# Performance work log

Measured on AMD Instinct MI355X. Metric: run time of the kernel, lower is better.

## Reference

```python
import jax, jax.numpy as jnp
import numpy as np

V, C, L, NH, NKV, HID, E, K, T, B = 32000, 1536, 2, 12, 4, 2048, 8, 2, 2048, 1
D = C // NH  # 128
NREP = NH // NKV
EPS = 1e-6

def _rms(x, w):
    return x * jax.lax.rsqrt(jnp.mean(x * x, axis=-1, keepdims=True) + EPS) * w


def setup_inputs() -> dict:
    key = jax.random.key(0)
    ks = jax.random.split(key, 14)
    s = 0.02
    inp = {
        "tokens": jax.random.randint(ks[0], (B, T), 0, V, dtype=jnp.int64),
        "emb": jax.random.normal(ks[1], (V, C), jnp.float32) * s,      # tied with output proj
        "pos": jax.random.normal(ks[2], (T, C), jnp.float32) * s,
        "wq": jax.random.normal(ks[3], (L, C, NH * D), jnp.float32) * s,
        "wk": jax.random.normal(ks[4], (L, C, NKV * D), jnp.float32) * s,
        "wv": jax.random.normal(ks[5], (L, C, NKV * D), jnp.float32) * s,
        "wo": jax.random.normal(ks[6], (L, C, C), jnp.float32) * s,
        "attn_norm_w": jnp.ones((L, C), jnp.float32),
        "ffn_norm_w": jnp.ones((L, C), jnp.float32),
        "gate": jax.random.normal(ks[7], (L, C, E), jnp.float32) * s,
        "ew1": jax.random.normal(ks[8], (L, E, C, HID), jnp.float32) * s,
        "ew2": jax.random.normal(ks[9], (L, E, HID, C), jnp.float32) * s,
        "ew3": jax.random.normal(ks[10], (L, E, C, HID), jnp.float32) * s,
        "final_norm_w": jnp.ones((C,), jnp.float32),
    }
    return inp


def _forward(tokens, emb, pos, wq, wk, wv, wo, attn_norm_w, ffn_norm_w, gate,
             ew1, ew2, ew3, final_norm_w):
    x = emb[tokens] + pos[None, :T]            # [B,T,C]; dropout=0 (eval)
    causal = jnp.tril(jnp.ones((T, T), bool))
    for l in range(L):
        # --- GQA attention ---
        h = _rms(x, attn_norm_w[l])
        q = (h @ wq[l]).reshape(B, T, NH, D).transpose(0, 2, 1, 3)     # [B,NH,T,D]
        k = (h @ wk[l]).reshape(B, T, NKV, D).transpose(0, 2, 1, 3)
        v = (h @ wv[l]).reshape(B, T, NKV, D).transpose(0, 2, 1, 3)
        k = jnp.repeat(k, NREP, axis=1)
        v = jnp.repeat(v, NREP, axis=1)
        scores = jnp.einsum("bhqd,bhkd->bhqk", q, k) / jnp.sqrt(jnp.float32(D))
        scores = jnp.where(causal, scores, jnp.finfo(scores.dtype).min)
        attn = jax.nn.softmax(scores, axis=-1)
        y = jnp.einsum("bhqk,bhkd->bhqd", attn, v)
        y = y.transpose(0, 2, 1, 3).reshape(B, T, C)
        x = x + y @ wo[l]
        # --- MoE FFN (top-k routed SwiGLU experts) ---
        xf = _rms(x, ffn_norm_w[l]).reshape(-1, C)                      # [N,C]
        probs = jax.nn.softmax(xf @ gate[l], axis=-1)                   # [N,E]
        topw, topi = jax.lax.top_k(probs, K)
        topw = topw / jnp.sum(topw, axis=-1, keepdims=True)
        dense_w = jnp.sum(jax.nn.one_hot(topi, E, dtype=xf.dtype) * topw[..., None], axis=1)  # [N,E]
        h1 = jnp.einsum("nc,ech->enh", xf, ew1[l])
        h3 = jnp.einsum("nc,ech->enh", xf, ew3[l])
        hh = jax.nn.silu(h1) * h3                                       # [E,N,HID]
        moe = jnp.einsum("ne,enh,ehc->nc", dense_w, hh, ew2[l])
        x = x + moe.reshape(B, T, C)
    x = _rms(x, final_norm_w)
    logits = x @ emb.T                                                   # tied output proj
    return logits


def reference(tokens, emb, pos, wq, wk, wv, wo, attn_norm_w, ffn_norm_w, gate,
              ew1, ew2, ew3, final_norm_w):
    return _forward(tokens, emb, pos, wq, wk, wv, wo, attn_norm_w, ffn_norm_w,
                    gate, ew1, ew2, ew3, final_norm_w)
```

## Files before the change

### kernel.cpp

```cpp
#include <hip/hip_runtime.h>
#include <hip/hip_bf16.h>
#include <math.h>

#define Tn   2048
#define Cn   1536
#define Vn   32000
#define NHn  12
#define NKVn 4
#define Dn   128
#define HIDn 2048
#define En   8
#define Kn   2
#define Ln   2
#define NREPn 3
#define EPSn 1e-6f
#define CHT  16
#define NCHn 4
#define QKVW 2560

using bf16 = __hip_bfloat16;
using bf16x8 = __attribute__((ext_vector_type(8))) short;
using f32x4v = __attribute__((ext_vector_type(4))) float;

__device__ __forceinline__ void split3(float v, short& h, short& m, short& lo) {
  bf16 b0 = __float2bfloat16(v);
  float r1 = v - __bfloat162float(b0);
  bf16 b1 = __float2bfloat16(r1);
  float r2 = r1 - __bfloat162float(b1);
  bf16 b2 = __float2bfloat16(r2);
  h = *reinterpret_cast<short*>(&b0);
  m = *reinterpret_cast<short*>(&b1);
  lo = *reinterpret_cast<short*>(&b2);
}
__device__ __forceinline__ float b2f(short s) {
  bf16 b = *reinterpret_cast<bf16*>(&s);
  return __bfloat162float(b);
}
__device__ __forceinline__ void gl_lds16(const void* g, void* l) {
  __builtin_amdgcn_global_load_lds((const __attribute__((address_space(1))) void*)g,
                                   (__attribute__((address_space(3))) void*)l, 16, 0, 0);
}

__global__ void embed_k(const int* __restrict__ tok, const float* __restrict__ emb,
                        const float* __restrict__ pos, float* __restrict__ x) {
  int n = blockIdx.x;
  int t = threadIdx.x;
  int id = tok[n];
  const float* er = emb + (size_t)id * Cn;
  const float* pr = pos + (size_t)n * Cn;
// ... 37 lines not shown
  const float* xr = x + (size_t)n * Cn;
  float v[6];
  float ss = 0.f;
#pragma unroll
  for (int i = 0; i < 6; i++) { v[i] = xr[t + i * 256]; ss += v[i] * v[i]; }
  for (int off = 32; off > 0; off >>= 1) ss += __shfl_down(ss, off, 64);
  __shared__ float red[4];
  __shared__ float rtot;
  int wave = t >> 6, lane = t & 63;
  if (lane == 0) red[wave] = ss;
  __syncthreads();
  if (t == 0) rtot = rsqrtf((red[0] + red[1] + red[2] + red[3]) / (float)Cn + EPSn);
  __syncthreads();
  float r = rtot;
#pragma unroll
  for (int i = 0; i < 6; i++) {
    int c = t + i * 256;
    float val = v[i] * r * w[c];
    size_t idx = (size_t)n * Cn + c;
    if (outf) outf[idx] = val;
    outb[idx] = __float2bfloat16(val);
  }
}

__global__ void f2b_k(const float* __restrict__ s, bf16* __restrict__ d, size_t n4) {
  size_t i = (size_t)blockIdx.x * 256 + threadIdx.x;
  size_t stride = (size_t)gridDim.x * 256;
  for (; i < n4; i += stride) {
    float4 v = ((const float4*)s)[i];
    d[i * 4 + 0] = __float2bfloat16(v.x);
    d[i * 4 + 1] = __float2bfloat16(v.y);
    d[i * 4 + 2] = __float2bfloat16(v.z);
    d[i * 4 + 3] = __float2bfloat16(v.w);
  }
}

__global__ void splita_k(const float* __restrict__ s, short* __restrict__ dh,
                         short* __restrict__ dm, short* __restrict__ dl, size_t n4) {
  size_t i = (size_t)blockIdx.x * 256 + threadIdx.x;
  size_t stride = (size_t)gridDim.x * 256;
  for (; i < n4; i += stride) {
    float4 v = ((const float4*)s)[i];
    float a[4] = {v.x, v.y, v.z, v.w};
#pragma unroll
    for (int u = 0; u < 4; u++) {
      short h, m, lo;
      split3(a[u], h, m, lo);
      dh[i * 4 + u] = h; dm[i * 4 + u] = m; dl[i * 4 + u] = lo;
    }
  }
}

__global__ void transp3_k(const float* __restrict__ src, short* __restrict__ dh,
                          short* __restrict__ dm, short* __restrict__ dl, int K, int N) {
  __shared__ __align__(16) float ls[32][33];
  size_t boff = (size_t)blockIdx.z * K * N;
  int k0 = blockIdx.x * 32, n0 = blockIdx.y * 32;
  int t = threadIdx.x;
  int kr = t >> 3, n4 = (t & 7) * 4;
  float4 vv = *(const float4*)&src[boff + (size_t)(k0 + kr) * N + n0 + n4];
  ls[kr][n4 + 0] = vv.x; ls[kr][n4 + 1] = vv.y; ls[kr][n4 + 2] = vv.z; ls[kr][n4 + 3] = vv.w;
  __syncthreads();
  int nr = t >> 3, k4 = (t & 7) * 4;
  size_t dbase = boff + (size_t)(n0 + nr) * K + k0 + k4;
#pragma unroll
  for (int u = 0; u < 4; u++) {
    short h, m, lo;
    split3(ls[k4 + u][nr], h, m, lo);
    dh[dbase + u] = h; dm[dbase + u] = m; dl[dbase + u] = lo;
  }
}

__global__ void transp_k(const float* __restrict__ src, bf16* __restrict__ dst, int K, int N) {
  __shared__ __align__(16) float ls[32][33];
  size_t boff = (size_t)blockIdx.z * K * N;
  int k0 = blockIdx.x * 32, n0 = blockIdx.y * 32;
  int t = threadIdx.x;
  int kr = t >> 3, n4 = (t & 7) * 4;
  float4 vv = *(const float4*)&src[boff + (size_t)(k0 + kr) * N + n0 + n4];
  ls[kr][n4 + 0] = vv.x; ls[kr][n4 + 1] = vv.y; ls[kr][n4 + 2] = vv.z; ls[kr][n4 + 3] = vv.w;
  __syncthreads();
  int nr = t >> 3, k4 = (t & 7) * 4;
// ... 106 lines not shown
      int ro = (wc + j * 16 + rl) * 32 + ko;
      bf16x8 bh = *(const bf16x8*)(sBH + ro);
      bf16x8 bm_ = *(const bf16x8*)(sBM + ro);
      bf16x8 bl = *(const bf16x8*)(sBL + ro);
#pragma unroll
      for (int i = 0; i < 4; i++) {
        acc[i][j] = __builtin_amdgcn_mfma_f32_16x16x32_bf16(aL[i], bh, acc[i][j], 0, 0, 0);
        acc[i][j] = __builtin_amdgcn_mfma_f32_16x16x32_bf16(aH[i], bl, acc[i][j], 0, 0, 0);
        acc[i][j] = __builtin_amdgcn_mfma_f32_16x16x32_bf16(aM[i], bm_, acc[i][j], 0, 0, 0);
        acc[i][j] = __builtin_amdgcn_mfma_f32_16x16x32_bf16(aM[i], bh, acc[i][j], 0, 0, 0);
        acc[i][j] = __builtin_amdgcn_mfma_f32_16x16x32_bf16(aH[i], bm_, acc[i][j], 0, 0, 0);
        acc[i][j] = __builtin_amdgcn_mfma_f32_16x16x32_bf16(aH[i], bh, acc[i][j], 0, 0, 0);
      }
    }
    __syncthreads();
  }
#pragma unroll
  for (int i = 0; i < 4; i++) {
    int rbase = bm + wr + i * 16 + (l >> 4) * 4;
#pragma unroll
    for (int j = 0; j < 4; j++) {
      int col = bn + wc + j * 16 + (l & 15);
#pragma unroll
      for (int r = 0; r < 4; r++) {
        size_t idx = (size_t)(rbase + r) * N + col;
        float v = acc[i][j][r];
        if (res) v += res[idx];
        Co[idx] = v;
      }
    }
  }
}

__global__ void __launch_bounds__(256) mexp6d(const bf16* __restrict__ AH, const bf16* __restrict__ AM,
                                              const bf16* __restrict__ AL,
                                              const bf16* __restrict__ B1H, const bf16* __restrict__ B1M,
                                              const bf16* __restrict__ B1L,
                                              const bf16* __restrict__ B3H, const bf16* __restrict__ B3M,
                                              const bf16* __restrict__ B3L,
                                              const int* __restrict__ perm, const int* __restrict__ cnt,
                                              int ebase,
                                              short* __restrict__ HH, short* __restrict__ HM,
                                              short* __restrict__ HL, int K, int N) {
  int e = ebase + blockIdx.z;
  int nrows = cnt[e];
  int bm = blockIdx.x * 128;
  if (bm >= nrows) return;
  int bn = blockIdx.y * 128;
  size_t eoff = (size_t)blockIdx.z * K * N;
  __shared__ __align__(16) bf16 sAH[128 * 32], sAM[128 * 32], sAL[128 * 32];
  __shared__ __align__(16) bf16 s1H[128 * 32], s1M[128 * 32], s1L[128 * 32];
  __shared__ __align__(16) bf16 s3H[128 * 32], s3M[128 * 32], s3L[128 * 32];
  __shared__ int prow[128];
  int t = threadIdx.x, l = t & 63, w = t >> 6;
  if (t < 128) {
    int i = bm + t;
    prow[t] = (i < nrows) ? perm[e * Tn + i] : -1;
  }
  __syncthreads();
  int wr = (w >> 1) * 64, wc = (w & 1) * 64;
  const f32x4v zero = {0.f, 0.f, 0.f, 0.f};
  f32x4v acc1[4][4], acc3[4][4];
#pragma unroll
  for (int i = 0; i < 4; i++)
#pragma unroll
    for (int j = 0; j < 4; j++) { acc1[i][j] = zero; acc3[i][j] = zero; }
  int p0 = prow[t >> 2], p1 = prow[64 + (t >> 2)];
  int g0r = (p0 >= 0) ? (p0 >> 1) : 0;
  int g1r = (p1 >= 0) ? (p1 >> 1) : 0;
  size_t a0 = (size_t)g0r * K + (t & 3) * 8;
  size_t a1 = (size_t)g1r * K + (t & 3) * 8;
  size_t b0 = eoff + (size_t)(bn + (t >> 2)) * K + (t & 3) * 8;
  size_t b1 = eoff + (size_t)(bn + 64 + (t >> 2)) * K + (t & 3) * 8;
  int rl = l & 15, ko = (l >> 4) * 8;
  for (int k0 = 0; k0 < K; k0 += 32) {
    gl_lds16(AH + a0 + k0, (char*)sAH + t * 16);
    gl_lds16(AH + a1 + k0, (char*)sAH + (256 + t) * 16);
    gl_lds16(AM + a0 + k0, (char*)sAM + t * 16);
    gl_lds16(AM + a1 + k0, (char*)sAM + (256 + t) * 16);
    gl_lds16(AL + a0 + k0, (char*)sAL + t * 16);
    gl_lds16(AL + a1 + k0, (char*)sAL + (256 + t) * 16);
    gl_lds16(B1H + b0 + k0, (char*)s1H + t * 16);
    gl_lds16(B1H + b1 + k0, (char*)s1H + (256 + t) * 16);
    gl_lds16(B1M + b0 + k0, (char*)s1M + t * 16);
    gl_lds16(B1M + b1 + k0, (char*)s1M + (256 + t) * 16);
    gl_lds16(B1L + b0 + k0, (char*)s1L + t * 16);
    gl_lds16(B1L + b1 + k0, (char*)s1L + (256 + t) * 16);
    gl_lds16(B3H + b0 + k0, (char*)s3H + t * 16);
    gl_lds16(B3H + b1 + k0, (char*)s3H + (256 + t) * 16);
    gl_lds16(B3M + b0 + k0, (char*)s3M + t * 16);
    gl_lds16(B3M + b1 + k0, (char*)s3M + (256 + t) * 16);
    gl_lds16(B3L + b0 + k0, (char*)s3L + t * 16);
    gl_lds16(B3L + b1 + k0, (char*)s3L + (256 + t) * 16);
    __syncthreads();
    bf16x8 aH[4], aM[4], aL[4];
#pragma unroll
    for (int i = 0; i < 4; i++) {
      int ro = (wr + i * 16 + rl) * 32 + ko;
      aH[i] = *(const bf16x8*)(sAH + ro);
      aM[i] = *(const bf16x8*)(sAM + ro);
      aL[i] = *(const bf16x8*)(sAL + ro);
    }
#pragma unroll
    for (int j = 0; j < 4; j++) {
      int ro = (wc + j * 16 + rl) * 32 + ko;
      bf16x8 bh = *(const bf16x8*)(s1H + ro);
      bf16x8 bm_ = *(const bf16x8*)(s1M + ro);
      bf16x8 bl = *(const bf16x8*)(s1L + ro);
#pragma unroll
      for (int i = 0; i < 4; i++) {
        acc1[i][j] = __builtin_amdgcn_mfma_f32_16x16x32_bf16(aL[i], bh, acc1[i][j], 0, 0, 0);
        acc1[i][j] = __builtin_amdgcn_mfma_f32_16x16x32_bf16(aH[i], bl, acc1[i][j], 0, 0, 0);
        acc1[i][j] = __builtin_amdgcn_mfma_f32_16x16x32_bf16(aM[i], bm_, acc1[i][j], 0, 0, 0);
        acc1[i][j] = __builtin_amdgcn_mfma_f32_16x16x32_bf16(aM[i], bh, acc1[i][j], 0, 0, 0);
        acc1[i][j] = __builtin_amdgcn_mfma_f32_16x16x32_bf16(aH[i], bm_, acc1[i][j], 0, 0, 0);
        acc1[i][j] = __builtin_amdgcn_mfma_f32_16x16x32_bf16(aH[i], bh, acc1[i][j], 0, 0, 0);
      }
      bh = *(const bf16x8*)(s3H + ro);
      bm_ = *(const bf16x8*)(s3M + ro);
      bl = *(const bf16x8*)(s3L + ro);
#pragma unroll
      for (int i = 0; i < 4; i++) {
        acc3[i][j] = __builtin_amdgcn_mfma_f32_16x16x32_bf16(aL[i], bh, acc3[i][j], 0, 0, 0);
        acc3[i][j] = __builtin_amdgcn_mfma_f32_16x16x32_bf16(aH[i], bl, acc3[i][j], 0, 0, 0);
        acc3[i][j] = __builtin_amdgcn_mfma_f32_16x16x32_bf16(aM[i], bm_, acc3[i][j], 0, 0, 0);
        acc3[i][j] = __builtin_amdgcn_mfma_f32_16x16x32_bf16(aM[i], bh, acc3[i][j], 0, 0, 0);
        acc3[i][j] = __builtin_amdgcn_mfma_f32_16x16x32_bf16(aH[i], bm_, acc3[i][j], 0, 0, 0);
        acc3[i][j] = __builtin_amdgcn_mfma_f32_16x16x32_bf16(aH[i], bh, acc3[i][j], 0, 0, 0);
      }
    }
    __syncthreads();
  }
#pragma unroll
  for (int i = 0; i < 4; i++) {
#pragma unroll
    for (int r = 0; r < 4; r++) {
      int lrow = wr + i * 16 + (l >> 4) * 4 + r;
      int p = prow[lrow];
      if (p < 0) continue;
#pragma unroll
      for (int j = 0; j < 4; j++) {
        int col = bn + wc + j * 16 + (l & 15);
        size_t idx = (size_t)p * N + col;
        float h1 = acc1[i][j][r], h3 = acc3[i][j][r];
        float hh = (h1 / (1.f + expf(-h1))) * h3;
        short h, m, lo;
        split3(hh, h, m, lo);
        HH[idx] = h; HM[idx] = m; HL[idx] = lo;
      }
    }
  }
}

__global__ void __launch_bounds__(256) mexp6(const bf16* __restrict__ AH, const bf16* __restrict__ AM,
                                             const bf16* __restrict__ AL,
                                             const bf16* __restrict__ BH, const bf16* __restrict__ BM,
                                             const bf16* __restrict__ BL,
                                             const int* __restrict__ perm, const int* __restrict__ cnt,
                                             int ebase, float* __restrict__ Co, int K, int N) {
  int e = ebase + blockIdx.z;
  int nrows = cnt[e];
  int bm = blockIdx.x * 128;
  if (bm >= nrows) return;
  int bn = blockIdx.y * 128;
  size_t eoff = (size_t)blockIdx.z * K * N;
  __shared__ __align__(16) bf16 sAH[128 * 32], sAM[128 * 32], sAL[128 * 32];
  __shared__ __align__(16) bf16 sBH[128 * 32], sBM[128 * 32], sBL[128 * 32];
  __shared__ int prow[128];
  int t = threadIdx.x, l = t & 63, w = t >> 6;
  if (t < 128) {
    int i = bm + t;
    prow[t] = (i < nrows) ? perm[e * Tn + i] : -1;
  }
  __syncthreads();
  int wr = (w >> 1) * 64, wc = (w & 1) * 64;
  const f32x4v zero = {0.f, 0.f, 0.f, 0.f};
  f32x4v acc[4][4];
#pragma unroll
  for (int i = 0; i < 4; i++)
#pragma unroll
    for (int j = 0; j < 4; j++) acc[i][j] = zero;
  int p0 = prow[t >> 2], p1 = prow[64 + (t >> 2)];
  int g0r = (p0 >= 0) ? p0 : 0;
  int g1r = (p1 >= 0) ? p1 : 0;
  size_t a0 = (size_t)g0r * K + (t & 3) * 8;
  size_t a1 = (size_t)g1r * K + (t & 3) * 8;
  size_t b0 = eoff + (size_t)(bn + (t >> 2)) * K + (t & 3) * 8;
  size_t b1 = eoff + (size_t)(bn + 64 + (t >> 2)) * K + (t & 3) * 8;
  int rl = l & 15, ko = (l >> 4) * 8;
  for (int k0 = 0; k0 < K; k0 += 32) {
    gl_lds16(AH + a0 + k0, (char*)sAH + t * 16);
    gl_lds16(AH + a1 + k0, (char*)sAH + (256 + t) * 16);
    gl_lds16(AM + a0 + k0, (char*)sAM + t * 16);
    gl_lds16(AM + a1 + k0, (char*)sAM + (256 + t) * 16);
    gl_lds16(AL + a0 + k0, (char*)sAL + t * 16);
    gl_lds16(AL + a1 + k0, (char*)sAL + (256 + t) * 16);
    gl_lds16(BH + b0 + k0, (char*)sBH + t * 16);
    gl_lds16(BH + b1 + k0, (char*)sBH + (256 + t) * 16);
    gl_lds16(BM + b0 + k0, (char*)sBM + t * 16);
    gl_lds16(BM + b1 + k0, (char*)sBM + (256 + t) * 16);
    gl_lds16(BL + b0 + k0, (char*)sBL + t * 16);
    gl_lds16(BL + b1 + k0, (char*)sBL + (256 + t) * 16);
    __syncthreads();
    bf16x8 aH[4], aM[4], aL[4];
#pragma unroll
    for (int i = 0; i < 4; i++) {
      int ro = (wr + i * 16 + rl) * 32 + ko;
      aH[i] = *(const bf16x8*)(sAH + ro);
      aM[i] = *(const bf16x8*)(sAM + ro);
      aL[i] = *(const bf16x8*)(sAL + ro);
    }
#pragma unroll
    for (int j = 0; j < 4; j++) {
      int ro = (wc + j * 16 + rl) * 32 + ko;
      bf16x8 bh = *(const bf16x8*)(sBH + ro);
      bf16x8 bm_ = *(const bf16x8*)(sBM + ro);
      bf16x8 bl = *(const bf16x8*)(sBL + ro);
#pragma unroll
      for (int i = 0; i < 4; i++) {
        acc[i][j] = __builtin_amdgcn_mfma_f32_16x16x32_bf16(aL[i], bh, acc[i][j], 0, 0, 0);
        acc[i][j] = __builtin_amdgcn_mfma_f32_16x16x32_bf16(aH[i], bl, acc[i][j], 0, 0, 0);
        acc[i][j] = __builtin_amdgcn_mfma_f32_16x16x32_bf16(aM[i], bm_, acc[i][j], 0, 0, 0);
        acc[i][j] = __builtin_amdgcn_mfma_f32_16x16x32_bf16(aM[i], bh, acc[i][j], 0, 0, 0);
        acc[i][j] = __builtin_amdgcn_mfma_f32_16x16x32_bf16(aH[i], bm_, acc[i][j], 0, 0, 0);
        acc[i][j] = __builtin_amdgcn_mfma_f32_16x16x32_bf16(aH[i], bh, acc[i][j], 0, 0, 0);
      }
    }
    __syncthreads();
  }
#pragma unroll
  for (int i = 0; i < 4; i++) {
#pragma unroll
    for (int r = 0; r < 4; r++) {
      int lrow = wr + i * 16 + (l >> 4) * 4 + r;
      int p = prow[lrow];
      if (p < 0) continue;
#pragma unroll
      for (int j = 0; j < 4; j++) {
        int col = bn + wc + j * 16 + (l & 15);
        Co[(size_t)p * N + col] = acc[i][j][r];
      }
    }
  }
}

__global__ void __launch_bounds__(256) mexpBd(const bf16* __restrict__ A, const bf16* __restrict__ B1,
                                              const bf16* __restrict__ B3,
                                              const int* __restrict__ perm, const int* __restrict__ cnt,
                                              int ebase, bf16* __restrict__ HB, int K, int N) {
  int e = ebase + blockIdx.z;
  int nrows = cnt[e];
  int bm = blockIdx.x * 128;
  if (bm >= nrows) return;
  int bn = blockIdx.y * 128;
  size_t eoff = (size_t)blockIdx.z * K * N;
  __shared__ __align__(16) bf16 sA[128 * 32];
  __shared__ __align__(16) bf16 s1[128 * 32];
  __shared__ __align__(16) bf16 s3[128 * 32];
  __shared__ int prow[128];
  int t = threadIdx.x, l = t & 63, w = t >> 6;
  if (t < 128) {
    int i = bm + t;
    prow[t] = (i < nrows) ? perm[e * Tn + i] : -1;
  }
  __syncthreads();
  int wr = (w >> 1) * 64, wc = (w & 1) * 64;
  const f32x4v zero = {0.f, 0.f, 0.f, 0.f};
  f32x4v acc1[4][4], acc3[4][4];
#pragma unroll
  for (int i = 0; i < 4; i++)
#pragma unroll
    for (int j = 0; j < 4; j++) { acc1[i][j] = zero; acc3[i][j] = zero; }
  int p0 = prow[t >> 2], p1 = prow[64 + (t >> 2)];
// ... 90 lines not shown
#pragma unroll
    for (int j = 0; j < 4; j++) b[j] = *(const bf16x8*)(sB + (wc + j * 16 + rl) * 32 + ko);
#pragma unroll
    for (int i = 0; i < 4; i++)
#pragma unroll
      for (int j = 0; j < 4; j++)
        acc[i][j] = __builtin_amdgcn_mfma_f32_16x16x32_bf16(a[i], b[j], acc[i][j], 0, 0, 0);
    __syncthreads();
  }
#pragma unroll
  for (int i = 0; i < 4; i++) {
#pragma unroll
    for (int r = 0; r < 4; r++) {
      int lrow = wr + i * 16 + (l >> 4) * 4 + r;
      int p = prow[lrow];
      if (p < 0) continue;
#pragma unroll
      for (int j = 0; j < 4; j++) {
        int col = bn + wc + j * 16 + (l & 15);
        Co[(size_t)p * N + col] = acc[i][j][r];
      }
    }
  }
}

__global__ void __launch_bounds__(256) attn_part_k(const float* __restrict__ qkv,
                                                   float* __restrict__ po,
                                                   float* __restrict__ pm,
                                                   float* __restrict__ pl) {
  int qt = blockIdx.x;
  int head = blockIdx.y;
  int ch = blockIdx.z;
  int ntiles = qt + 1;
  int tA = ch * CHT;
  if (tA >= ntiles) return;
  int tB = tA + CHT < ntiles ? tA + CHT : ntiles;
  int kvh = head / NREPn;
  int q0 = qt * 32;
  int t = threadIdx.x;
  int r = t >> 3, g = t & 7, d0 = g * 16;
  int row = q0 + r;
  __shared__ __align__(16) float ks[32][Dn + 4];
  __shared__ __align__(16) float vs[32][Dn + 4];
  const float scale = 0.08838834764831845f;
  float qr[16];
  {
    const float* qrow = qkv + (size_t)row * QKVW + head * Dn + d0;
#pragma unroll
    for (int j = 0; j < 16; j += 4) {
      float4 u = *(const float4*)(qrow + j);
      qr[j] = u.x * scale; qr[j + 1] = u.y * scale;
      qr[j + 2] = u.z * scale; qr[j + 3] = u.w * scale;
    }
  }
  float o[16];
#pragma unroll
  for (int j = 0; j < 16; j++) o[j] = 0.f;
  float rowm = -1e30f, rowl = 0.f;

  for (int kt = tA; kt < tB; kt++) {
    int kv0 = kt * 32;
    for (int e = t; e < 32 * 32; e += 256) {
      int rr = e >> 5, c4 = (e & 31) * 4;
      size_t base = (size_t)(kv0 + rr) * QKVW + kvh * Dn + c4;
      *(float4*)&ks[rr][c4] = *(const float4*)(qkv + base + 1536);
      *(float4*)&vs[rr][c4] = *(const float4*)(qkv + base + 2048);
    }
    __syncthreads();
    float s[32];
#pragma unroll
    for (int kk = 0; kk < 32; kk++) {
      const float* krow = &ks[kk][d0];
      float p = 0.f;
#pragma unroll
// ... 5 lines not shown
      p += __shfl_xor(p, 2);
      p += __shfl_xor(p, 4);
      s[kk] = p;
    }
    if (kt == qt) {
#pragma unroll
      for (int kk = 0; kk < 32; kk++)
        if (kk > r) s[kk] = -1e30f;
    }
    float mx = s[0];
#pragma unroll
    for (int kk = 1; kk < 32; kk++) mx = fmaxf(mx, s[kk]);
    float m_new = fmaxf(rowm, mx);
    float corr = expf(rowm - m_new);
    float sum = 0.f;
#pragma unroll
    for (int kk = 0; kk < 32; kk++) { s[kk] = expf(s[kk] - m_new); sum += s[kk]; }
    rowl = rowl * corr + sum;
    rowm = m_new;
#pragma unroll
    for (int j = 0; j < 16; j++) o[j] *= corr;
#pragma unroll
    for (int kk = 0; kk < 32; kk++) {
      float p = s[kk];
      const float* vrow = &vs[kk][d0];
#pragma unroll
      for (int j = 0; j < 16; j += 4) {
        float4 u = *(const float4*)(vrow + j);
        o[j] += p * u.x; o[j + 1] += p * u.y; o[j + 2] += p * u.z; o[j + 3] += p * u.w;
      }
    }
    __syncthreads();
  }
  size_t pidx = ((size_t)head * Tn + row) * NCHn + ch;
  if (g == 0) { pm[pidx] = rowm; pl[pidx] = rowl; }
  float* porow = po + pidx * Dn + d0;
#pragma unroll
  for (int j = 0; j < 16; j += 4) {
    float4 u;
    u.x = o[j]; u.y = o[j + 1]; u.z = o[j + 2]; u.w = o[j + 3];
    *(float4*)(porow + j) = u;
  }
}

__global__ void __launch_bounds__(256) attn_merge_k(const float* __restrict__ po,
                                                    const float* __restrict__ pm,
                                                    const float* __restrict__ pl,
                                                    float* __restrict__ y) {
  int qt = blockIdx.x;
  int head = blockIdx.y;
  int q0 = qt * 32;
  int t = threadIdx.x;
  int r = t >> 3, g = t & 7, d0 = g * 16;
  int row = q0 + r;
  int nach = (qt + CHT) / CHT;
  size_t base = ((size_t)head * Tn + row) * NCHn;
  float M = -1e30f;
  for (int c = 0; c < nach; c++) M = fmaxf(M, pm[base + c]);
  float L = 0.f;
  float acc[16];
#pragma unroll
  for (int j = 0; j < 16; j++) acc[j] = 0.f;
  for (int c = 0; c < nach; c++) {
    float wgt = expf(pm[base + c] - M);
    L += pl[base + c] * wgt;
    const float* p = po + (base + c) * Dn + d0;
#pragma unroll
    for (int j = 0; j < 16; j += 4) {
      float4 u = *(const float4*)(p + j);
      acc[j] += wgt * u.x; acc[j + 1] += wgt * u.y;
      acc[j + 2] += wgt * u.z; acc[j + 3] += wgt * u.w;
    }
  }
  float inv = 1.f / L;
  float* yrow = y + (size_t)row * (NHn * Dn) + head * Dn + d0;
#pragma unroll
  for (int j = 0; j < 16; j += 4) {
    float4 u;
    u.x = acc[j] * inv; u.y = acc[j + 1] * inv;
    u.z = acc[j + 2] * inv; u.w = acc[j + 3] * inv;
    *(float4*)(yrow + j) = u;
  }
}

__global__ void gate_k(const float* __restrict__ xf, const float* __restrict__ g,
                       float* __restrict__ gl) {
  int n = blockIdx.x, t = threadIdx.x;
  int e = t & 7, cs = t >> 3;
  const float* xr = xf + (size_t)n * Cn;
  float s = 0.f;
  for (int j = 0; j < Cn / 32; j++) {
    int c = cs + 32 * j;
    s += xr[c] * g[c * En + e];
  }
  __shared__ float red[256];
  red[t] = s;
  __syncthreads();
  if (t < 8) {
    float tot = 0.f;
    for (int j = 0; j < 32; j++) tot += red[t + 8 * j];
    gl[n * En + t] = tot;
  }
}

__global__ void route_k(const float* __restrict__ gl, float* __restrict__ topw,
                        int* __restrict__ cnt, int* __restrict__ perm) {
  int n = blockIdx.x * blockDim.x + threadIdx.x;
  if (n >= Tn) return;
  float p[En];
  float mx = -1e30f;
#pragma unroll
  for (int e = 0; e < En; e++) { p[e] = gl[n * En + e]; mx = fmaxf(mx, p[e]); }
  float s = 0.f;
#pragma unroll
// ... 52 lines not shown
    off = (off + 255) & ~(size_t)255;
    size_t p = off;
    off += bytes;
    return p;
  };
  size_t o_x    = alloc(NC * 4);
  size_t o_h    = alloc(NC * 4);
  size_t o_gl   = alloc((size_t)Tn * En * 4);
  size_t o_topw = alloc((size_t)Tn * Kn * 4);
  size_t o_cnt  = alloc(64);
  size_t o_perm = alloc((size_t)En * Tn * 4);
  size_t wlvl   = (size_t)4 * Cn * HIDn * 2;
  size_t o_w    = alloc(3 * wlvl);
  size_t hs_lvl = NC * 2;
  size_t o_hs   = alloc(3 * hs_lvl);
  size_t o_qkv  = alloc((size_t)Tn * QKVW * 4);
  size_t o_yb   = alloc(NC * 4);
  size_t hb_lvl = (size_t)Tn * Kn * HIDn * 2;
  size_t o_hbs  = o_qkv;
  size_t end_hbs = o_hbs + 3 * hb_lvl;
  if (off < end_hbs) off = end_hbs;
  size_t o_pair = alloc(NC * 4);
  size_t o_po   = alloc((size_t)NHn * Tn * NCHn * Dn * 4);
  size_t o_pm   = alloc((size_t)NHn * Tn * NCHn * 4);
  size_t o_pl   = alloc((size_t)NHn * Tn * NCHn * 4);

  float* x       = (float*)(wsb + o_x);
  float* h       = (float*)(wsb + o_h);
  float* gl      = (float*)(wsb + o_gl);
  float* topw    = (float*)(wsb + o_topw);
  int*   cnt     = (int*)(wsb + o_cnt);
  int*   perm    = (int*)(wsb + o_perm);
  float* qkvb    = (float*)(wsb + o_qkv);
  float* yb      = (float*)(wsb + o_yb);
  float* pairout = (float*)(wsb + o_pair);
  bf16*  hb      = (bf16*)(wsb + o_pair);
  bf16*  embB    = (bf16*)(wsb + o_w);
  float* po      = (float*)(wsb + o_po);
  float* pm      = (float*)(wsb + o_pm);
  float* pl      = (float*)(wsb + o_pl);

  short* hs[3]; short* hbs[3];
  for (int s = 0; s < 3; s++) {
    hs[s]  = (short*)(wsb + o_hs + (size_t)s * hs_lvl);
    hbs[s] = (short*)(wsb + o_hbs + (size_t)s * hb_lvl);
  }
  size_t qkvw_lvl = (size_t)QKVW * Cn * 2;
  size_t wo_lvl   = (size_t)Cn * Cn * 2;
  short* qkvT[3]; short* woT[3];
  for (int s = 0; s < 3; s++) {
    qkvT[s] = (short*)(wsb + o_w + (size_t)s * qkvw_lvl);
    woT[s]  = (short*)(wsb + o_w + 3 * qkvw_lvl + (size_t)s * wo_lvl);
  }
  size_t q2lvl = (size_t)2 * Cn * HIDn * 2;
  short* e1T[3]; short* e3T[3]; short* e2T[3];
  for (int s = 0; s < 3; s++) {
    e1T[s] = (short*)(wsb + o_w + (size_t)s * q2lvl);
    e3T[s] = (short*)(wsb + o_w + 3 * q2lvl + (size_t)s * q2lvl);
    e2T[s] = (short*)(wsb + o_w + (size_t)s * wlvl);
  }
  bf16* ew1B = (bf16*)(wsb + o_w);
  bf16* ew3B = (bf16*)(wsb + o_w + wlvl);
  bf16* ew2B = (bf16*)(wsb + o_w);

  embed_k<<<Tn, 256, 0, stream>>>(tokens, emb, pos, x);
  for (int l = 0; l < Ln; l++) {
    const float* wq_l = wq + (size_t)l * Cn * (NHn * Dn);
    const float* wk_l = wk + (size_t)l * Cn * (NKVn * Dn);
    const float* wv_l = wv + (size_t)l * Cn * (NKVn * Dn);
    const float* wo_l = wo + (size_t)l * Cn * Cn;
    const float* g_l  = gate + (size_t)l * Cn * En;
    const float* e1_l = ew1 + (size_t)l * En * Cn * HIDn;
    const float* e2_l = ew2 + (size_t)l * En * HIDn * Cn;
    const float* e3_l = ew3 + (size_t)l * En * Cn * HIDn;

    transp3_k<<<dim3(Cn / 32, (NHn * Dn) / 32, 1), 256, 0, stream>>>(wq_l, qkvT[0], qkvT[1], qkvT[2], Cn, NHn * Dn);
    transp3_k<<<dim3(Cn / 32, (NKVn * Dn) / 32, 1), 256, 0, stream>>>(
        wk_l, qkvT[0] + (size_t)1536 * Cn, qkvT[1] + (size_t)1536 * Cn, qkvT[2] + (size_t)1536 * Cn, Cn, NKVn * Dn);
    transp3_k<<<dim3(Cn / 32, (NKVn * Dn) / 32, 1), 256, 0, stream>>>(
        wv_l, qkvT[0] + (size_t)2048 * Cn, qkvT[1] + (size_t)2048 * Cn, qkvT[2] + (size_t)2048 * Cn, Cn, NKVn * Dn);
    transp3_k<<<dim3(Cn / 32, Cn / 32, 1), 256, 0, stream>>>(wo_l, woT[0], woT[1], woT[2], Cn, Cn);
    rms3_k<<<Tn, 256, 0, stream>>>(x, attn_nw + (size_t)l * Cn, nullptr, hs[0], hs[1], hs[2]);
    gemm6<<<dim3(Tn / 128, QKVW / 128), 256, 0, stream>>>(
        (bf16*)hs[0], (bf16*)hs[1], (bf16*)hs[2], (bf16*)qkvT[0], (bf16*)qkvT[1], (bf16*)qkvT[2],
        nullptr, qkvb, Tn, QKVW, Cn);
    attn_part_k<<<dim3(Tn / 32, NHn, NCHn), 256, 0, stream>>>(qkvb, po, pm, pl);
    attn_merge_k<<<dim3(Tn / 32, NHn), 256, 0, stream>>>(po, pm, pl, yb);
    splita_k<<<2048, 256, 0, stream>>>(yb, hs[0], hs[1], hs[2], NC / 4);
    gemm6<<<dim3(Tn / 128, Cn / 128), 256, 0, stream>>>(
        (bf16*)hs[0], (bf16*)hs[1], (bf16*)hs[2], (bf16*)woT[0], (bf16*)woT[1], (bf16*)woT[2],
        x, x, Tn, Cn, Cn);

    if (l < Ln - 1) {
      rms3_k<<<Tn, 256, 0, stream>>>(x, ffn_nw + (size_t)l * Cn, h, hs[0], hs[1], hs[2]);
      gate_k<<<Tn, 256, 0, stream>>>(h, g_l, gl);
      hipMemsetAsync(cnt, 0, 64, stream);
      route_k<<<Tn / 256, 256, 0, stream>>>(gl, topw, cnt, perm);
      for (int q = 0; q < 4; q++) {
        size_t qoff = (size_t)q * 2 * Cn * HIDn;
        transp3_k<<<dim3(Cn / 32, HIDn / 32, 2), 256, 0, stream>>>(e1_l + qoff, e1T[0], e1T[1], e1T[2], Cn, HIDn);
        transp3_k<<<dim3(Cn / 32, HIDn / 32, 2), 256, 0, stream>>>(e3_l + qoff, e3T[0], e3T[1], e3T[2], Cn, HIDn);
        mexp6d<<<dim3(Tn / 128, HIDn / 128, 2), 256, 0, stream>>>(
            (bf16*)hs[0], (bf16*)hs[1], (bf16*)hs[2],
            (bf16*)e1T[0], (bf16*)e1T[1], (bf16*)e1T[2],
            (bf16*)e3T[0], (bf16*)e3T[1], (bf16*)e3T[2],
            perm, cnt, q * 2, hbs[0], hbs[1], hbs[2], Cn, HIDn);
      }
      for (int half = 0; half < 2; half++) {
        size_t hoff = (size_t)half * 4 * HIDn * Cn;
        transp3_k<<<dim3(HIDn / 32, Cn / 32, 4), 256, 0, stream>>>(e2_l + hoff, e2T[0], e2T[1], e2T[2], HIDn, Cn);
        mexp6<<<dim3(Tn / 128, Cn / 128, 4), 256, 0, stream>>>(
            (bf16*)hbs[0], (bf16*)hbs[1], (bf16*)hbs[2], (bf16*)e2T[0], (bf16*)e2T[1], (bf16*)e2T[2],
            perm, cnt, half * 4, pairout, HIDn, Cn);
      }
    } else {
      bf16* hbf = (bf16*)hs[0];
      bf16* hbB = (bf16*)hbs[0];
      rmsb_k<<<Tn, 256, 0, stream>>>(x, ffn_nw + (size_t)l * Cn, h, hbf);
      gate_k<<<Tn, 256, 0, stream>>>(h, g_l, gl);
      hipMemsetAsync(cnt, 0, 64, stream);
      route_k<<<Tn / 256, 256, 0, stream>>>(gl, topw, cnt, perm);
      for (int half = 0; half < 2; half++) {
        size_t hoff = (size_t)half * 4 * Cn * HIDn;
        int eb = half * 4;
        transp_k<<<dim3(Cn / 32, HIDn / 32, 4), 256, 0, stream>>>(e1_l + hoff, ew1B, Cn, HIDn);
        transp_k<<<dim3(Cn / 32, HIDn / 32, 4), 256, 0, stream>>>(e3_l + hoff, ew3B, Cn, HIDn);
        mexpBd<<<dim3(Tn / 128, HIDn / 128, 4), 256, 0, stream>>>(
            hbf, ew1B, ew3B, perm, cnt, eb, hbB, Cn, HIDn);
        transp_k<<<dim3(HIDn / 32, Cn / 32, 4), 256, 0, stream>>>(e2_l + (size_t)half * 4 * HIDn * Cn, ew2B, HIDn, Cn);
        mexpB<<<dim3(Tn / 128, Cn / 128, 4), 256, 0, stream>>>(
            hbB, ew2B, perm, cnt, eb, pairout, HIDn, Cn);
      }
    }
    combine_k<<<Tn, 256, 0, stream>>>(pairout, topw, x);
  }
  rmsb_k<<<Tn, 256, 0, stream>>>(x, final_nw, nullptr, hb);
  f2b_k<<<2048, 256, 0, stream>>>(emb, embB, (size_t)Vn * Cn / 4);
  gemm_btl<<<dim3(Tn / 128, Vn / 128), 256, 0, stream>>>(hb, embB, nullptr, out, Tn, Vn, Cn);
}
```

Baseline: 5.360 ms.

## Split fused dual-GEMM expert kernel, rebalance attention chunks, fuse merge with split

Removes the fused W1/W3 expert kernel (mexp6d) and replaces it with two passes of a generalized mexp6 kernel. The first pass stores the split h1, and the second reads it back and applies SiLU gating in the epilogue. Expert processing moves from quarter groups of two experts to halves of four, so there are fewer transposes and larger launches, at the cost of an extra round trip of h1 through memory. Attention partial chunks are now balanced evenly across NCH splits instead of fixed 16-tile chunks. The attention merge writes the three-way bf16 split directly, removing the separate fp32 output buffer and the splita pass.

```diff
diff --git a/kernel.cpp b/kernel.cpp
--- a/kernel.cpp
+++ b/kernel.cpp
@@ -14,7 +14,6 @@
 #define Ln   2
 #define NREPn 3
 #define EPSn 1e-6f
-#define CHT  16
 #define NCHn 4
 #define QKVW 2560
 
@@ -118,22 +117,6 @@
     d[i * 4 + 1] = __float2bfloat16(v.y);
     d[i * 4 + 2] = __float2bfloat16(v.z);
     d[i * 4 + 3] = __float2bfloat16(v.w);
-  }
-}
-
-__global__ void splita_k(const float* __restrict__ s, short* __restrict__ dh,
-                         short* __restrict__ dm, short* __restrict__ dl, size_t n4) {
-  size_t i = (size_t)blockIdx.x * 256 + threadIdx.x;
-  size_t stride = (size_t)gridDim.x * 256;
-  for (; i < n4; i += stride) {
-    float4 v = ((const float4*)s)[i];
-    float a[4] = {v.x, v.y, v.z, v.w};
-#pragma unroll
-    for (int u = 0; u < 4; u++) {
-      short h, m, lo;
-      split3(a[u], h, m, lo);
-      dh[i * 4 + u] = h; dm[i * 4 + u] = m; dl[i * 4 + u] = lo;
-    }
   }
 }
 
@@ -306,132 +289,15 @@
   }
 }
 
-__global__ void __launch_bounds__(256) mexp6d(const bf16* __restrict__ AH, const bf16* __restrict__ AM,
-                                              const bf16* __restrict__ AL,
-                                              const bf16* __restrict__ B1H, const bf16* __restrict__ B1M,
-                                              const bf16* __restrict__ B1L,
-                                              const bf16* __restrict__ B3H, const bf16* __restrict__ B3M,
-                                              const bf16* __restrict__ B3L,
-                                              const int* __restrict__ perm, const int* __restrict__ cnt,
-                                              int ebase,
-                                              short* __restrict__ HH, short* __restrict__ HM,
-                                              short* __restrict__ HL, int K, int N) {
-  int e = ebase + blockIdx.z;
-  int nrows = cnt[e];
-  int bm = blockIdx.x * 128;
-  if (bm >= nrows) return;
-  int bn = blockIdx.y * 128;
-  size_t eoff = (size_t)blockIdx.z * K * N;
-  __shared__ __align__(16) bf16 sAH[128 * 32], sAM[128 * 32], sAL[128 * 32];
-  __shared__ __align__(16) bf16 s1H[128 * 32], s1M[128 * 32], s1L[128 * 32];
-  __shared__ __align__(16) bf16 s3H[128 * 32], s3M[128 * 32], s3L[128 * 32];
-  __shared__ int prow[128];
-  int t = threadIdx.x, l = t & 63, w = t >> 6;
-  if (t < 128) {
-    int i = bm + t;
-    prow[t] = (i < nrows) ? perm[e * Tn + i] : -1;
-  }
-  __syncthreads();
-  int wr = (w >> 1) * 64, wc = (w & 1) * 64;
-  const f32x4v zero = {0.f, 0.f, 0.f, 0.f};
-  f32x4v acc1[4][4], acc3[4][4];
-#pragma unroll
-  for (int i = 0; i < 4; i++)
-#pragma unroll
-    for (int j = 0; j < 4; j++) { acc1[i][j] = zero; acc3[i][j] = zero; }
-  int p0 = prow[t >> 2], p1 = prow[64 + (t >> 2)];
-  int g0r = (p0 >= 0) ? (p0 >> 1) : 0;
-  int g1r = (p1 >= 0) ? (p1 >> 1) : 0;
-  size_t a0 = (size_t)g0r * K + (t & 3) * 8;
-  size_t a1 = (size_t)g1r * K + (t & 3) * 8;
-  size_t b0 = eoff + (size_t)(bn + (t >> 2)) * K + (t & 3) * 8;
-  size_t b1 = eoff + (size_t)(bn + 64 + (t >> 2)) * K + (t & 3) * 8;
-  int rl = l & 15, ko = (l >> 4) * 8;
-  for (int k0 = 0; k0 < K; k0 += 32) {
-    gl_lds16(AH + a0 + k0, (char*)sAH + t * 16);
-    gl_lds16(AH + a1 + k0, (char*)sAH + (256 + t) * 16);
-    gl_lds16(AM + a0 + k0, (char*)sAM + t * 16);
-    gl_lds16(AM + a1 + k0, (char*)sAM + (256 + t) * 16);
-    gl_lds16(AL + a0 + k0, (char*)sAL + t * 16);
-    gl_lds16(AL + a1 + k0, (char*)sAL + (256 + t) * 16);
-    gl_lds16(B1H + b0 + k0, (char*)s1H + t * 16);
-    gl_lds16(B1H + b1 + k0, (char*)s1H + (256 + t) * 16);
-    gl_lds16(B1M + b0 + k0, (char*)s1M + t * 16);
-    gl_lds16(B1M + b1 + k0, (char*)s1M + (256 + t) * 16);
-    gl_lds16(B1L + b0 + k0, (char*)s1L + t * 16);
-    gl_lds16(B1L + b1 + k0, (char*)s1L + (256 + t) * 16);
-    gl_lds16(B3H + b0 + k0, (char*)s3H + t * 16);
-    gl_lds16(B3H + b1 + k0, (char*)s3H + (256 + t) * 16);
-    gl_lds16(B3M + b0 + k0, (char*)s3M + t * 16);
-    gl_lds16(B3M + b1 + k0, (char*)s3M + (256 + t) * 16);
-    gl_lds16(B3L + b0 + k0, (char*)s3L + t * 16);
-    gl_lds16(B3L + b1 + k0, (char*)s3L + (256 + t) * 16);
-    __syncthreads();
-    bf16x8 aH[4], aM[4], aL[4];
-#pragma unroll
-    for (int i = 0; i < 4; i++) {
-      int ro = (wr + i * 16 + rl) * 32 + ko;
-      aH[i] = *(const bf16x8*)(sAH + ro);
-      aM[i] = *(const bf16x8*)(sAM + ro);
-      aL[i] = *(const bf16x8*)(sAL + ro);
-    }
-#pragma unroll
-    for (int j = 0; j < 4; j++) {
-      int ro = (wc + j * 16 + rl) * 32 + ko;
-      bf16x8 bh = *(const bf16x8*)(s1H + ro);
-      bf16x8 bm_ = *(const bf16x8*)(s1M + ro);
-      bf16x8 bl = *(const bf16x8*)(s1L + ro);
-#pragma unroll
-      for (int i = 0; i < 4; i++) {
-        acc1[i][j] = __builtin_amdgcn_mfma_f32_16x16x32_bf16(aL[i], bh, acc1[i][j], 0, 0, 0);
-        acc1[i][j] = __builtin_amdgcn_mfma_f32_16x16x32_bf16(aH[i], bl, acc1[i][j], 0, 0, 0);
-        acc1[i][j] = __builtin_amdgcn_mfma_f32_16x16x32_bf16(aM[i], bm_, acc1[i][j], 0, 0, 0);
-        acc1[i][j] = __builtin_amdgcn_mfma_f32_16x16x32_bf16(aM[i], bh, acc1[i][j], 0, 0, 0);
-        acc1[i][j] = __builtin_amdgcn_mfma_f32_16x16x32_bf16(aH[i], bm_, acc1[i][j], 0, 0, 0);
-        acc1[i][j] = __builtin_amdgcn_mfma_f32_16x16x32_bf16(aH[i], bh, acc1[i][j], 0, 0, 0);
-      }
-      bh = *(const bf16x8*)(s3H + ro);
-      bm_ = *(const bf16x8*)(s3M + ro);
-      bl = *(const bf16x8*)(s3L + ro);
-#pragma unroll
-      for (int i = 0; i < 4; i++) {
-        acc3[i][j] = __builtin_amdgcn_mfma_f32_16x16x32_bf16(aL[i], bh, acc3[i][j], 0, 0, 0);
-        acc3[i][j] = __builtin_amdgcn_mfma_f32_16x16x32_bf16(aH[i], bl, acc3[i][j], 0, 0, 0);
-        acc3[i][j] = __builtin_amdgcn_mfma_f32_16x16x32_bf16(aM[i], bm_, acc3[i][j], 0, 0, 0);
-        acc3[i][j] = __builtin_amdgcn_mfma_f32_16x16x32_bf16(aM[i], bh, acc3[i][j], 0, 0, 0);
-        acc3[i][j] = __builtin_amdgcn_mfma_f32_16x16x32_bf16(aH[i], bm_, acc3[i][j], 0, 0, 0);
-        acc3[i][j] = __builtin_amdgcn_mfma_f32_16x16x32_bf16(aH[i], bh, acc3[i][j], 0, 0, 0);
-      }
-    }
-    __syncthreads();
-  }
-#pragma unroll
-  for (int i = 0; i < 4; i++) {
-#pragma unroll
-    for (int r = 0; r < 4; r++) {
-      int lrow = wr + i * 16 + (l >> 4) * 4 + r;
-      int p = prow[lrow];
-      if (p < 0) continue;
-#pragma unroll
-      for (int j = 0; j < 4; j++) {
-        int col = bn + wc + j * 16 + (l & 15);
-        size_t idx = (size_t)p * N + col;
-        float h1 = acc1[i][j][r], h3 = acc3[i][j][r];
-        float hh = (h1 / (1.f + expf(-h1))) * h3;
-        short h, m, lo;
-        split3(hh, h, m, lo);
-        HH[idx] = h; HM[idx] = m; HL[idx] = lo;
-      }
-    }
-  }
-}
-
 __global__ void __launch_bounds__(256) mexp6(const bf16* __restrict__ AH, const bf16* __restrict__ AM,
                                              const bf16* __restrict__ AL,
                                              const bf16* __restrict__ BH, const bf16* __restrict__ BM,
                                              const bf16* __restrict__ BL,
                                              const int* __restrict__ perm, const int* __restrict__ cnt,
-                                             int ebase, float* __restrict__ Co, int K, int N) {
+                                             int ebase,
+                                             short* __restrict__ HH, short* __restrict__ HM,
+                                             short* __restrict__ HL,
+                                             float* __restrict__ Co, int K, int N, int mode) {
   int e = ebase + blockIdx.z;
   int nrows = cnt[e];
   int bm = blockIdx.x * 128;
@@ -455,8 +321,8 @@
 #pragma unroll
     for (int j = 0; j < 4; j++) acc[i][j] = zero;
   int p0 = prow[t >> 2], p1 = prow[64 + (t >> 2)];
-  int g0r = (p0 >= 0) ? p0 : 0;
-  int g1r = (p1 >= 0) ? p1 : 0;
+  int g0r = (p0 >= 0) ? (mode == 2 ? p0 : (p0 >> 1)) : 0;
+  int g1r = (p1 >= 0) ? (mode == 2 ? p1 : (p1 >> 1)) : 0;
   size_t a0 = (size_t)g0r * K + (t & 3) * 8;
   size_t a1 = (size_t)g1r * K + (t & 3) * 8;
   size_t b0 = eoff + (size_t)(bn + (t >> 2)) * K + (t & 3) * 8;
@@ -512,7 +378,21 @@
 #pragma unroll
       for (int j = 0; j < 4; j++) {
         int col = bn + wc + j * 16 + (l & 15);
-        Co[(size_t)p * N + col] = acc[i][j][r];
+        size_t idx = (size_t)p * N + col;
+        float v = acc[i][j][r];
+        if (mode == 0) {
+          short h, m, lo;
+          split3(v, h, m, lo);
+          HH[idx] = h; HM[idx] = m; HL[idx] = lo;
+        } else if (mode == 1) {
+          float v1 = b2f(HH[idx]) + b2f(HM[idx]) + b2f(HL[idx]);
+          float hh = (v1 / (1.f + expf(-v1))) * v;
+          short h, m, lo;
+          split3(hh, h, m, lo);
+          HH[idx] = h; HM[idx] = m; HL[idx] = lo;
+        } else {
+          Co[idx] = v;
+        }
       }
     }
   }
@@ -669,14 +549,24 @@
   int head = blockIdx.y;
   int ch = blockIdx.z;
   int ntiles = qt + 1;
-  int tA = ch * CHT;
-  if (tA >= ntiles) return;
-  int tB = tA + CHT < ntiles ? tA + CHT : ntiles;
-  int kvh = head / NREPn;
-  int q0 = qt * 32;
+  int tA = (ch * ntiles) / NCHn;
+  int tB = ((ch + 1) * ntiles) / NCHn;
   int t = threadIdx.x;
   int r = t >> 3, g = t & 7, d0 = g * 16;
+  int q0 = qt * 32;
   int row = q0 + r;
+  size_t pidx = ((size_t)head * Tn + row) * NCHn + ch;
+  if (tA >= tB) {
+    if (g == 0) { pm[pidx] = -1e30f; pl[pidx] = 0.f; }
+    float* porow = po + pidx * Dn + d0;
+#pragma unroll
+    for (int j = 0; j < 16; j += 4) {
+      float4 z = {0.f, 0.f, 0.f, 0.f};
+      *(float4*)(porow + j) = z;
+    }
+    return;
+  }
+  int kvh = head / NREPn;
   __shared__ __align__(16) float ks[32][Dn + 4];
   __shared__ __align__(16) float vs[32][Dn + 4];
   const float scale = 0.08838834764831845f;
@@ -748,7 +638,6 @@
     }
     __syncthreads();
   }
-  size_t pidx = ((size_t)head * Tn + row) * NCHn + ch;
   if (g == 0) { pm[pidx] = rowm; pl[pidx] = rowl; }
   float* porow = po + pidx * Dn + d0;
 #pragma unroll
@@ -759,25 +648,28 @@
   }
 }
 
-__global__ void __launch_bounds__(256) attn_merge_k(const float* __restrict__ po,
-                                                    const float* __restrict__ pm,
-                                                    const float* __restrict__ pl,
-                                                    float* __restrict__ y) {
+__global__ void __launch_bounds__(256) attn_merge3_k(const float* __restrict__ po,
+                                                     const float* __restrict__ pm,
+                                                     const float* __restrict__ pl,
+                                                     short* __restrict__ dh,
+                                                     short* __restrict__ dm,
+                                                     short* __restrict__ dl) {
   int qt = blockIdx.x;
   int head = blockIdx.y;
   int q0 = qt * 32;
   int t = threadIdx.x;
   int r = t >> 3, g = t & 7, d0 = g * 16;
   int row = q0 + r;
-  int nach = (qt + CHT) / CHT;
   size_t base = ((size_t)head * Tn + row) * NCHn;
   float M = -1e30f;
-  for (int c = 0; c < nach; c++) M = fmaxf(M, pm[base + c]);
+#pragma unroll
+  for (int c = 0; c < NCHn; c++) M = fmaxf(M, pm[base + c]);
   float L = 0.f;
   float acc[16];
 #pragma unroll
   for (int j = 0; j < 16; j++) acc[j] = 0.f;
-  for (int c = 0; c < nach; c++) {
+#pragma unroll
+  for (int c = 0; c < NCHn; c++) {
     float wgt = expf(pm[base + c] - M);
     L += pl[base + c] * wgt;
     const float* p = po + (base + c) * Dn + d0;
@@ -789,13 +681,12 @@
     }
   }
   float inv = 1.f / L;
-  float* yrow = y + (size_t)row * (NHn * Dn) + head * Dn + d0;
-#pragma unroll
-  for (int j = 0; j < 16; j += 4) {
-    float4 u;
-    u.x = acc[j] * inv; u.y = acc[j + 1] * inv;
-    u.z = acc[j + 2] * inv; u.w = acc[j + 3] * inv;
-    *(float4*)(yrow + j) = u;
+  size_t yidx = (size_t)row * Cn + head * Dn + d0;
+#pragma unroll
+  for (int j = 0; j < 16; j++) {
+    short h, m, lo;
+    split3(acc[j] * inv, h, m, lo);
+    dh[yidx + j] = h; dm[yidx + j] = m; dl[yidx + j] = lo;
   }
 }
 
@@ -914,7 +805,6 @@
   int*   cnt     = (int*)(wsb + o_cnt);
   int*   perm    = (int*)(wsb + o_perm);
   float* qkvb    = (float*)(wsb + o_qkv);
-  float* yb      = (float*)(wsb + o_yb);
   float* pairout = (float*)(wsb + o_pair);
   bf16*  hb      = (bf16*)(wsb + o_pair);
   bf16*  embB    = (bf16*)(wsb + o_w);
@@ -922,10 +812,11 @@
   float* pm      = (float*)(wsb + o_pm);
   float* pl      = (float*)(wsb + o_pl);
 
-  short* hs[3]; short* hbs[3];
+  short* hs[3]; short* hbs[3]; short* ewT[3];
   for (int s = 0; s < 3; s++) {
     hs[s]  = (short*)(wsb + o_hs + (size_t)s * hs_lvl);
     hbs[s] = (short*)(wsb + o_hbs + (size_t)s * hb_lvl);
+    ewT[s] = (short*)(wsb + o_w + (size_t)s * wlvl);
   }
   size_t qkvw_lvl = (size_t)QKVW * Cn * 2;
   size_t wo_lvl   = (size_t)Cn * Cn * 2;
@@ -933,13 +824,6 @@
   for (int s = 0; s < 3; s++) {
     qkvT[s] = (short*)(wsb + o_w + (size_t)s * qkvw_lvl);
     woT[s]  = (short*)(wsb + o_w + 3 * qkvw_lvl + (size_t)s * wo_lvl);
-  }
-  size_t q2lvl = (size_t)2 * Cn * HIDn * 2;
-  short* e1T[3]; short* e3T[3]; short* e2T[3];
-  for (int s = 0; s < 3; s++) {
-    e1T[s] = (short*)(wsb + o_w + (size_t)s * q2lvl);
-    e3T[s] = (short*)(wsb + o_w + 3 * q2lvl + (size_t)s * q2lvl);
-    e2T[s] = (short*)(wsb + o_w + (size_t)s * wlvl);
   }
   bf16* ew1B = (bf16*)(wsb + o_w);
   bf16* ew3B = (bf16*)(wsb + o_w + wlvl);
@@ -967,8 +851,7 @@
         (bf16*)hs[0], (bf16*)hs[1], (bf16*)hs[2], (bf16*)qkvT[0], (bf16*)qkvT[1], (bf16*)qkvT[2],
         nullptr, qkvb, Tn, QKVW, Cn);
     attn_part_k<<<dim3(Tn / 32, NHn, NCHn), 256, 0, stream>>>(qkvb, po, pm, pl);
-    attn_merge_k<<<dim3(Tn / 32, NHn), 256, 0, stream>>>(po, pm, pl, yb);
-    splita_k<<<2048, 256, 0, stream>>>(yb, hs[0], hs[1], hs[2], NC / 4);
+    attn_merge3_k<<<dim3(Tn / 32, NHn), 256, 0, stream>>>(po, pm, pl, hs[0], hs[1], hs[2]);
     gemm6<<<dim3(Tn / 128, Cn / 128), 256, 0, stream>>>(
         (bf16*)hs[0], (bf16*)hs[1], (bf16*)hs[2], (bf16*)woT[0], (bf16*)woT[1], (bf16*)woT[2],
         x, x, Tn, Cn, Cn);
@@ -978,22 +861,21 @@
       gate_k<<<Tn, 256, 0, stream>>>(h, g_l, gl);
       hipMemsetAsync(cnt, 0, 64, stream);
       route_k<<<Tn / 256, 256, 0, stream>>>(gl, topw, cnt, perm);
-      for (int q = 0; q < 4; q++) {
-        size_t qoff = (size_t)q * 2 * Cn * HIDn;
-        transp3_k<<<dim3(Cn / 32, HIDn / 32, 2), 256, 0, stream>>>(e1_l + qoff, e1T[0], e1T[1], e1T[2], Cn, HIDn);
-        transp3_k<<<dim3(Cn / 32, HIDn / 32, 2), 256, 0, stream>>>(e3_l + qoff, e3T[0], e3T[1], e3T[2], Cn, HIDn);
-        mexp6d<<<dim3(Tn / 128, HIDn / 128, 2), 256, 0, stream>>>(
-            (bf16*)hs[0], (bf16*)hs[1], (bf16*)hs[2],
-            (bf16*)e1T[0], (bf16*)e1T[1], (bf16*)e1T[2],
-            (bf16*)e3T[0], (bf16*)e3T[1], (bf16*)e3T[2],
-            perm, cnt, q * 2, hbs[0], hbs[1], hbs[2], Cn, HIDn);
-      }
       for (int half = 0; half < 2; half++) {
-        size_t hoff = (size_t)half * 4 * HIDn * Cn;
-        transp3_k<<<dim3(HIDn / 32, Cn / 32, 4), 256, 0, stream>>>(e2_l + hoff, e2T[0], e2T[1], e2T[2], HIDn, Cn);
+        size_t hoff = (size_t)half * 4 * Cn * HIDn;
+        int eb = half * 4;
+        transp3_k<<<dim3(Cn / 32, HIDn / 32, 4), 256, 0, stream>>>(e1_l + hoff, ewT[0], ewT[1], ewT[2], Cn, HIDn);
+        mexp6<<<dim3(Tn / 128, HIDn / 128, 4), 256, 0, stream>>>(
+            (bf16*)hs[0], (bf16*)hs[1], (bf16*)hs[2], (bf16*)ewT[0], (bf16*)ewT[1], (bf16*)ewT[2],
+            perm, cnt, eb, hbs[0], hbs[1], hbs[2], nullptr, Cn, HIDn, 0);
+        transp3_k<<<dim3(Cn / 32, HIDn / 32, 4), 256, 0, stream>>>(e3_l + hoff, ewT[0], ewT[1], ewT[2], Cn, HIDn);
+        mexp6<<<dim3(Tn / 128, HIDn / 128, 4), 256, 0, stream>>>(
+            (bf16*)hs[0], (bf16*)hs[1], (bf16*)hs[2], (bf16*)ewT[0], (bf16*)ewT[1], (bf16*)ewT[2],
+            perm, cnt, eb, hbs[0], hbs[1], hbs[2], nullptr, Cn, HIDn, 1);
+        transp3_k<<<dim3(HIDn / 32, Cn / 32, 4), 256, 0, stream>>>(e2_l + (size_t)half * 4 * HIDn * Cn, ewT[0], ewT[1], ewT[2], HIDn, Cn);
         mexp6<<<dim3(Tn / 128, Cn / 128, 4), 256, 0, stream>>>(
-            (bf16*)hbs[0], (bf16*)hbs[1], (bf16*)hbs[2], (bf16*)e2T[0], (bf16*)e2T[1], (bf16*)e2T[2],
-            perm, cnt, half * 4, pairout, HIDn, Cn);
+            (bf16*)hbs[0], (bf16*)hbs[1], (bf16*)hbs[2], (bf16*)ewT[0], (bf16*)ewT[1], (bf16*)ewT[2],
+            perm, cnt, eb, hbs[0], hbs[1], hbs[2], pairout, HIDn, Cn, 2);
       }
     } else {
       bf16* hbf = (bf16*)hs[0];
```

Result: faster. 5.114 ms (-4.6%).
